# Kernel optimization log

Hardware: AMD Instinct MI355X
Metric: run time of the kernel (lower is better)

## Reference

```python
import jax, jax.numpy as jnp
import numpy as np

DIM = 256; H = 64; W = 64; NH = 8; NL = 1; NP = 8; HD = DIM // NH
B = 4


def _bilinear(img, grid):
    """torch.grid_sample(mode='bilinear', padding='zeros', align_corners=False).
    img: [C, Hl, Wl]; grid: [N, P, 2] normalized xy in [-1, 1]. Returns [C, N, P]."""
    Hl, Wl = img.shape[1], img.shape[2]
    x = (grid[..., 0] + 1.0) * (Wl * 0.5) - 0.5
    y = (grid[..., 1] + 1.0) * (Hl * 0.5) - 0.5
    x0 = jnp.floor(x); y0 = jnp.floor(y)
    wx = x - x0; wy = y - y0

    def gather(xi, yi):
        valid = (xi >= 0) & (xi < Wl) & (yi >= 0) & (yi < Hl)
        xc = jnp.clip(xi, 0, Wl - 1).astype(jnp.int32)
        yc = jnp.clip(yi, 0, Hl - 1).astype(jnp.int32)
        return img[:, yc, xc] * valid.astype(img.dtype)[None]  # [C, N, P]

    v00 = gather(x0, y0); v01 = gather(x0 + 1, y0)
    v10 = gather(x0, y0 + 1); v11 = gather(x0 + 1, y0 + 1)
    top = v00 * (1.0 - wx) + v01 * wx
    bot = v10 * (1.0 - wx) + v11 * wx
    return top * (1.0 - wy) + bot * wy


def _msda(value, loc, att):
    """multi_scale_deformable_attn_pytorch.
    value: [b, nv, NH, HD]; loc: [b, nq, NH, NL, NP, 2] in [0,1]; att: [b, nq, NH, NL, NP]."""
    b, nv, _, _ = value.shape
    nq = loc.shape[1]
    grids = 2.0 * loc - 1.0
    bn = b * NH
    level_shapes = [(H, W)] * NL  # all levels share the single [H, W] grid here
    sampled_levels = []
    offset = 0
    for l, (Hl, Wl) in enumerate(level_shapes):
        vl = value[:, offset:offset + Hl * Wl]                     # [b, HW, NH, HD]
        offset += Hl * Wl
        vl = vl.transpose(0, 2, 3, 1).reshape(bn, HD, Hl, Wl)      # [b*NH, HD, Hl, Wl]
        gl = grids[:, :, :, l].transpose(0, 2, 1, 3, 4).reshape(bn, nq, NP, 2)
        sampled_levels.append(jax.vmap(_bilinear)(vl, gl))         # [b*NH, HD, nq, NP]
    sampled = jnp.stack(sampled_levels, axis=3)                    # [b*NH, HD, nq, NL, NP]
    w = att.transpose(0, 2, 1, 3, 4).reshape(bn, 1, nq, NL, NP)
    out = jnp.sum(sampled * w, axis=(3, 4))                        # [b*NH, HD, nq]
    return out.reshape(b, NH, HD, nq).transpose(0, 3, 1, 2).reshape(b, nq, NH * HD)


def _forward(query, value, W_loc, b_loc, W_att, b_att, W_val, b_val, W_out, b_out):
    b = query.shape[0]
    nq = H * W
    q = query.transpose(0, 2, 3, 1).reshape(b, nq, DIM)
    v = value.transpose(0, 2, 3, 1).reshape(b, nq, DIM)
    loc = (q @ W_loc.T + b_loc).reshape(b, nq, NH, NL, NP, 2)
    att = jax.nn.softmax((q @ W_att.T + b_att).reshape(b, nq, NH, NL * NP), axis=-1)
    att = att.reshape(b, nq, NH, NL, NP)
    v = (v @ W_val.T + b_val).reshape(b, nq, NH, HD)
    out = _msda(v, loc, att)                                       # [b, nq, DIM]
    return out @ W_out.T + b_out


def setup_inputs() -> dict:
    key = jax.random.key(0)
    ks = jax.random.split(key, 12)
    s = 0.02
    return {
        "query": jax.random.normal(ks[0], (B, DIM, H, W), jnp.float32),
        "value": jax.random.normal(ks[1], (B, DIM, H, W), jnp.float32),
        "W_loc": jax.random.normal(ks[2], (NH * NL * NP * 2, DIM), jnp.float32) * s,
        "b_loc": jax.random.normal(ks[3], (NH * NL * NP * 2,), jnp.float32) * s,
        "W_att": jax.random.normal(ks[4], (NH * NL * NP, DIM), jnp.float32) * s,
        "b_att": jax.random.normal(ks[5], (NH * NL * NP,), jnp.float32) * s,
        "W_val": jax.random.normal(ks[6], (DIM, DIM), jnp.float32) * s,
        "b_val": jax.random.normal(ks[7], (DIM,), jnp.float32) * s,
        "W_out": jax.random.normal(ks[8], (DIM, DIM), jnp.float32) * s,
        "b_out": jax.random.normal(ks[9], (DIM,), jnp.float32) * s,
    }


def reference(query, value, W_loc, b_loc, W_att, b_att, W_val, b_val, W_out, b_out):
    return _forward(query, value, W_loc, b_loc, W_att, b_att, W_val, b_val, W_out, b_out)
```

## Files before the change

kernel.cpp:

```cpp
#include <hip/hip_runtime.h>
#include <hip/hip_bf16.h>
#include <math.h>

#define NQ   4096
#define DIMC 256
#define NHC  8
#define NPC  8
#define HDC  32
#define HC   64
#define WC   64
#define BC   4
#define LSTR 40

typedef __bf16 bf16x8 __attribute__((ext_vector_type(8)));
typedef __attribute__((ext_vector_type(4))) float f4;
typedef __attribute__((ext_vector_type(8))) short s8v;

__device__ __forceinline__ ushort f2bf(float f) {
  __hip_bfloat16 h = __float2bfloat16(f);
  union { __hip_bfloat16 h; ushort u; } c; c.h = h; return c.u;
}
__device__ __forceinline__ float bfu2f(ushort u) {
  union { unsigned i; float f; } c; c.i = ((unsigned)u) << 16; return c.f;
}
__device__ __forceinline__ float bflo(unsigned u) {
  union { unsigned i; float f; } c; c.i = u << 16; return c.f;
}
__device__ __forceinline__ float bfhi(unsigned u) {
  union { unsigned i; float f; } c; c.i = u & 0xffff0000u; return c.f;
}

union bfr8 { ushort u[8]; bf16x8 v; s8v s; };

__global__ __launch_bounds__(256) void k_proj(
    const float* __restrict__ query, const float* __restrict__ value,
    const float* __restrict__ W_loc, const float* __restrict__ b_loc,
    const float* __restrict__ W_att, const float* __restrict__ b_att,
    const float* __restrict__ W_val, const float* __restrict__ b_val,
    float* __restrict__ loc, float* __restrict__ att,
    ushort* __restrict__ vproj) {
  __shared__ __align__(16) ushort smem[4 * 64 * LSTR];
  const int tid = threadIdx.x;
  const int b = blockIdx.z, n0 = blockIdx.x * 64;
  const int lane = tid & 63, wid = tid >> 6;
  const int wn0 = (wid & 1) * 32, wo0 = (wid >> 1) * 32;
  const int am = lane & 15, kq = (lane >> 4) * 8;
  const int an = tid & 63, ak = (tid >> 6) * 8;
  const int wo = tid >> 2, wk = (tid & 3) * 8;

  f4 acc[2][2];
#pragma unroll
  for (int mi = 0; mi < 2; ++mi) { acc[mi][0] = (f4)0.f; acc[mi][1] = (f4)0.f; }

  if (blockIdx.y < 3) {
    ushort* Ah = smem;
    ushort* Al = smem + 64 * LSTR;
    ushort* Wh = smem + 2 * 64 * LSTR;
    ushort* Wl = smem + 3 * 64 * LSTR;
    const int o0 = blockIdx.y * 64;
    const float* Xb = query + (size_t)b * DIMC * NQ + n0 + an;
    const int oo = o0 + wo;
    const float* Wrow = (oo < 128) ? (W_loc + (size_t)oo * DIMC)
                                   : (W_att + (size_t)(oo - 128) * DIMC);
    float ax[8];
    float4 wx0, wx1;
#pragma unroll
    for (int j = 0; j < 8; ++j) ax[j] = Xb[(size_t)(ak + j) * NQ];
    wx0 = *(const float4*)(Wrow + wk);
    wx1 = *(const float4*)(Wrow + wk + 4);

    for (int t = 0; t < 8; ++t) {
      __syncthreads();
      {
        bfr8 ph, pl;
#pragma unroll
        for (int j = 0; j < 8; ++j) {
          ushort h = f2bf(ax[j]);
          ph.u[j] = h;
          pl.u[j] = f2bf(ax[j] - bfu2f(h));
        }
        *(s8v*)(&Ah[an * LSTR + ak]) = ph.s;
        *(s8v*)(&Al[an * LSTR + ak]) = pl.s;
        float wt[8] = {wx0.x, wx0.y, wx0.z, wx0.w, wx1.x, wx1.y, wx1.z, wx1.w};
        bfr8 qh, ql;
#pragma unroll
        for (int j = 0; j < 8; ++j) {
          ushort h = f2bf(wt[j]);
          qh.u[j] = h;
          ql.u[j] = f2bf(wt[j] - bfu2f(h));
        }
        *(s8v*)(&Wh[wo * LSTR + wk]) = qh.s;
        *(s8v*)(&Wl[wo * LSTR + wk]) = ql.s;
      }
      if (t < 7) {
        const int k0 = (t + 1) * 32;
#pragma unroll
        for (int j = 0; j < 8; ++j) ax[j] = Xb[(size_t)(k0 + ak + j) * NQ];
        wx0 = *(const float4*)(Wrow + k0 + wk);
        wx1 = *(const float4*)(Wrow + k0 + wk + 4);
      }
      __syncthreads();
      bf16x8 ah[2], al[2], bh[2], bl[2];
#pragma unroll
      for (int mi = 0; mi < 2; ++mi) {
        ah[mi] = *(const bf16x8*)(&Ah[(wn0 + mi * 16 + am) * LSTR + kq]);
        al[mi] = *(const bf16x8*)(&Al[(wn0 + mi * 16 + am) * LSTR + kq]);
      }
#pragma unroll
      for (int oj = 0; oj < 2; ++oj) {
        bh[oj] = *(const bf16x8*)(&Wh[(wo0 + oj * 16 + am) * LSTR + kq]);
        bl[oj] = *(const bf16x8*)(&Wl[(wo0 + oj * 16 + am) * LSTR + kq]);
      }
#pragma unroll
      for (int mi = 0; mi < 2; ++mi)
#pragma unroll
        for (int oj = 0; oj < 2; ++oj) {
          acc[mi][oj] = __builtin_amdgcn_mfma_f32_16x16x32_bf16(ah[mi], bh[oj], acc[mi][oj], 0, 0, 0);
          acc[mi][oj] = __builtin_amdgcn_mfma_f32_16x16x32_bf16(al[mi], bh[oj], acc[mi][oj], 0, 0, 0);
          acc[mi][oj] = __builtin_amdgcn_mfma_f32_16x16x32_bf16(ah[mi], bl[oj], acc[mi][oj], 0, 0, 0);
        }
    }
    const int o0l = blockIdx.y * 64;
    const bool isAtt = (o0l >= 128);
    float* dstBase = isAtt ? att : loc;
    const float* bias = isAtt ? b_att : b_loc;
    const int ostride = isAtt ? 64 : 128;
    const int ob = isAtt ? o0l - 128 : o0l;
#pragma unroll
    for (int oj = 0; oj < 2; ++oj) {
      const int o = ob + wo0 + oj * 16 + am;
      const float bv = bias[o];
#pragma unroll
      for (int mi = 0; mi < 2; ++mi) {
        const int nb = n0 + wn0 + mi * 16 + (lane >> 4) * 4;
#pragma unroll
        for (int r = 0; r < 4; ++r)
          dstBase[((size_t)b * NQ + nb + r) * ostride + o] = acc[mi][oj][r] + bv;
      }
    }
  } else {
    ushort* As = smem;
    ushort* Ws = smem + 64 * LSTR;
    const int o0 = (blockIdx.y - 3) * 64;
    const float* Xb = value + (size_t)b * DIMC * NQ + n0 + an;
    const float* Wrow = W_val + (size_t)(o0 + wo) * DIMC;

    float ax[8];
    float4 wx0, wx1;
#pragma unroll
    for (int j = 0; j < 8; ++j) ax[j] = Xb[(size_t)(ak + j) * NQ];
    wx0 = *(const float4*)(Wrow + wk);
    wx1 = *(const float4*)(Wrow + wk + 4);

    for (int t = 0; t < 8; ++t) {
      __syncthreads();
      {
        bfr8 pa;
#pragma unroll
        for (int j = 0; j < 8; ++j) pa.u[j] = f2bf(ax[j]);
        *(s8v*)(&As[an * LSTR + ak]) = pa.s;
        float wt[8] = {wx0.x, wx0.y, wx0.z, wx0.w, wx1.x, wx1.y, wx1.z, wx1.w};
        bfr8 pw;
#pragma unroll
        for (int j = 0; j < 8; ++j) pw.u[j] = f2bf(wt[j]);
        *(s8v*)(&Ws[wo * LSTR + wk]) = pw.s;
      }
      if (t < 7) {
        const int k0 = (t + 1) * 32;
#pragma unroll
        for (int j = 0; j < 8; ++j) ax[j] = Xb[(size_t)(k0 + ak + j) * NQ];
        wx0 = *(const float4*)(Wrow + k0 + wk);
        wx1 = *(const float4*)(Wrow + k0 + wk + 4);
      }
      __syncthreads();
      bf16x8 af[2], bf[2];
#pragma unroll
      for (int mi = 0; mi < 2; ++mi)
        af[mi] = *(const bf16x8*)(&As[(wn0 + mi * 16 + am) * LSTR + kq]);
#pragma unroll
      for (int oj = 0; oj < 2; ++oj)
        bf[oj] = *(const bf16x8*)(&Ws[(wo0 + oj * 16 + am) * LSTR + kq]);
#pragma unroll
      for (int mi = 0; mi < 2; ++mi)
#pragma unroll
        for (int oj = 0; oj < 2; ++oj)
          acc[mi][oj] = __builtin_amdgcn_mfma_f32_16x16x32_bf16(af[mi], bf[oj], acc[mi][oj], 0, 0, 0);
    }
#pragma unroll
    for (int oj = 0; oj < 2; ++oj) {
      const int o = o0 + wo0 + oj * 16 + am;
      const int h = o >> 5, d = o & 31;
      const float bias = b_val[o];
      ushort* dst = vproj + ((size_t)(b * NHC + h) * NQ) * HDC + d;
#pragma unroll
      for (int mi = 0; mi < 2; ++mi) {
        const int nb = n0 + wn0 + mi * 16 + (lane >> 4) * 4;
#pragma unroll
        for (int r = 0; r < 4; ++r)
          dst[(size_t)(nb + r) * HDC] = f2bf(acc[mi][oj][r] + bias);
      }
    }
  }
}

__global__ __launch_bounds__(256) void k_sample(
    const float* __restrict__ loc, const float* __restrict__ attL,
    const ushort* __restrict__ vproj, ushort* __restrict__ msda) {
  __shared__ float4 Lc[64][9];
  __shared__ int4   Lo[64][9];
  const int b = blockIdx.z, h = blockIdx.y;
  const int tid = threadIdx.x;
  const int n0 = blockIdx.x * 64;
#pragma unroll
  for (int it = 0; it < 2; ++it) {
    const int idx = it * 256 + tid;
    const int q = idx >> 3, p = idx & 7;
    const int n = n0 + q;
    const float lg = attL[((size_t)b * NQ + n) * 64 + h * 8 + p];
    float m = lg;
#pragma unroll
    for (int off = 1; off < 8; off <<= 1) m = fmaxf(m, __shfl_xor(m, off, 64));
    const float e = __expf(lg - m);
    float s = e;
#pragma unroll
    for (int off = 1; off < 8; off <<= 1) s += __shfl_xor(s, off, 64);
    const float w = e / s;
    const float2 xy = *(const float2*)(loc + ((size_t)b * NQ + n) * 128 + h * 16 + p * 2);
    const float x = xy.x * 64.0f - 0.5f;
    const float y = xy.y * 64.0f - 0.5f;
    const float x0f = floorf(x), y0f = floorf(y);
    const float wx = x - x0f, wy = y - y0f;
    const int x0 = (int)x0f, y0 = (int)y0f;
    const int x1 = x0 + 1, y1 = y0 + 1;
    const float fx0 = (x0 >= 0 && x0 < WC) ? 1.f : 0.f;
    const float fx1 = (x1 >= 0 && x1 < WC) ? 1.f : 0.f;
    const float fy0 = (y0 >= 0 && y0 < HC) ? 1.f : 0.f;
    const float fy1 = (y1 >= 0 && y1 < HC) ? 1.f : 0.f;
    const int cx0 = min(max(x0, 0), WC - 1), cx1 = min(max(x1, 0), WC - 1);
    const int cy0 = min(max(y0, 0), HC - 1), cy1 = min(max(y1, 0), HC - 1);
    float4 cf;
    cf.x = w * (1.f - wx) * (1.f - wy) * fx0 * fy0;
    cf.y = w * wx * (1.f - wy) * fx1 * fy0;
    cf.z = w * (1.f - wx) * wy * fx0 * fy1;
    cf.w = w * wx * wy * fx1 * fy1;
    int4 of;
    of.x = (cy0 * WC + cx0) * HDC; of.y = (cy0 * WC + cx1) * HDC;
    of.z = (cy1 * WC + cx0) * HDC; of.w = (cy1 * WC + cx1) * HDC;
    Lc[q][p] = cf; Lo[q][p] = of;
  }
  __syncthreads();
  const int q = tid >> 2, d8 = (tid & 3) * 8;
  const int n = n0 + q;
  const ushort* vb = vproj + (size_t)((b * NHC + h) * NQ) * HDC + d8;
  float a[8] = {};
#pragma unroll
  for (int p = 0; p < 8; ++p) {
    const int4 of = Lo[q][p];
    const float4 cf = Lc[q][p];
    const uint4 u00 = *(const uint4*)(vb + of.x);
    const uint4 u01 = *(const uint4*)(vb + of.y);
    const uint4 u10 = *(const uint4*)(vb + of.z);
    const uint4 u11 = *(const uint4*)(vb + of.w);
    const unsigned c00[4] = {u00.x, u00.y, u00.z, u00.w};
    const unsigned c01[4] = {u01.x, u01.y, u01.z, u01.w};
    const unsigned c10[4] = {u10.x, u10.y, u10.z, u10.w};
    const unsigned c11[4] = {u11.x, u11.y, u11.z, u11.w};
#pragma unroll
    for (int j = 0; j < 4; ++j) {
      a[2 * j]     += cf.x * bflo(c00[j]) + cf.y * bflo(c01[j]) + cf.z * bflo(c10[j]) + cf.w * bflo(c11[j]);
      a[2 * j + 1] += cf.x * bfhi(c00[j]) + cf.y * bfhi(c01[j]) + cf.z * bfhi(c10[j]) + cf.w * bfhi(c11[j]);
    }
  }
  bfr8 r;
#pragma unroll
  for (int j = 0; j < 8; ++j) r.u[j] = f2bf(a[j]);
  *(s8v*)(msda + ((size_t)b * NQ + n) * DIMC + h * HDC + d8) = r.s;
}

__global__ __launch_bounds__(256) void k_out(
    const ushort* __restrict__ msda, const float* __restrict__ W_out,
    const float* __restrict__ b_out, float* __restrict__ out) {
  __shared__ __align__(16) ushort As[64 * LSTR];
  __shared__ __align__(16) ushort Ws[64 * LSTR];
  const int b = blockIdx.z, n0 = blockIdx.x * 64, o0 = blockIdx.y * 64;
  const int tid = threadIdx.x, lane = tid & 63, wid = tid >> 6;
  const int wn0 = (wid & 1) * 32, wo0 = (wid >> 1) * 32;
  const int am = lane & 15, kq = (lane >> 4) * 8;
  const int ar = tid >> 2, akq = (tid & 3) * 8;
  const int wo = tid >> 2, wk = (tid & 3) * 8;
  const ushort* Ab = msda + ((size_t)b * NQ + n0 + ar) * DIMC + akq;
  const float* Wrow = W_out + (size_t)(o0 + wo) * DIMC;

  f4 acc[2][2];
#pragma unroll
  for (int mi = 0; mi < 2; ++mi) { acc[mi][0] = (f4)0.f; acc[mi][1] = (f4)0.f; }

  s8v aval = *(const s8v*)(Ab);
  float4 wx0 = *(const float4*)(Wrow + wk);
  float4 wx1 = *(const float4*)(Wrow + wk + 4);

  for (int t = 0; t < 8; ++t) {
    __syncthreads();
    *(s8v*)(&As[ar * LSTR + akq]) = aval;
    {
      float wt[8] = {wx0.x, wx0.y, wx0.z, wx0.w, wx1.x, wx1.y, wx1.z, wx1.w};
      bfr8 pw;
#pragma unroll
      for (int j = 0; j < 8; ++j) pw.u[j] = f2bf(wt[j]);
      *(s8v*)(&Ws[wo * LSTR + wk]) = pw.s;
    }
    if (t < 7) {
      const int k0 = (t + 1) * 32;
      aval = *(const s8v*)(Ab + k0);
      wx0 = *(const float4*)(Wrow + k0 + wk);
      wx1 = *(const float4*)(Wrow + k0 + wk + 4);
    }
    __syncthreads();
    bf16x8 af[2], bf[2];
#pragma unroll
    for (int mi = 0; mi < 2; ++mi)
      af[mi] = *(const bf16x8*)(&As[(wn0 + mi * 16 + am) * LSTR + kq]);
#pragma unroll
    for (int oj = 0; oj < 2; ++oj)
      bf[oj] = *(const bf16x8*)(&Ws[(wo0 + oj * 16 + am) * LSTR + kq]);
#pragma unroll
    for (int mi = 0; mi < 2; ++mi)
#pragma unroll
      for (int oj = 0; oj < 2; ++oj)
        acc[mi][oj] = __builtin_amdgcn_mfma_f32_16x16x32_bf16(af[mi], bf[oj], acc[mi][oj], 0, 0, 0);
  }
#pragma unroll
  for (int oj = 0; oj < 2; ++oj) {
    const int o = o0 + wo0 + oj * 16 + am;
    const float bias = b_out[o];
#pragma unroll
    for (int mi = 0; mi < 2; ++mi) {
      const int nb = n0 + wn0 + mi * 16 + (lane >> 4) * 4;
#pragma unroll
      for (int r = 0; r < 4; ++r)
        out[((size_t)b * NQ + nb + r) * DIMC + o] = acc[mi][oj][r] + bias;
    }
  }
}

extern "C" void kernel_launch(void* const* d_in, const int* in_sizes, int n_in,
                              void* d_out, int out_size, void* d_ws, size_t ws_size,
                              hipStream_t stream) {
  const float* query = (const float*)d_in[0];
  const float* value = (const float*)d_in[1];
  const float* W_loc = (const float*)d_in[2];
  const float* b_loc = (const float*)d_in[3];
  const float* W_att = (const float*)d_in[4];
  const float* b_att = (const float*)d_in[5];
  const float* W_val = (const float*)d_in[6];
  const float* b_val = (const float*)d_in[7];
  const float* W_out = (const float*)d_in[8];
  const float* b_out = (const float*)d_in[9];
  float* out = (float*)d_out;

  float* ws = (float*)d_ws;
  float* loc    = ws;
  float* att    = loc + (size_t)BC * NQ * 128;
  ushort* vproj = (ushort*)(att + (size_t)BC * NQ * 64);
  ushort* msda  = vproj + (size_t)BC * NHC * NQ * HDC;

  dim3 blk(256);
  k_proj  <<<dim3(NQ / 64, 7, BC), blk, 0, stream>>>(query, value, W_loc, b_loc,
             W_att, b_att, W_val, b_val, loc, att, vproj);
  k_sample<<<dim3(NQ / 64, NHC, BC), blk, 0, stream>>>(loc, att, vproj, msda);
  k_out   <<<dim3(NQ / 64, 4, BC), blk, 0, stream>>>(msda, W_out, b_out, out);
}
```

Baseline: 127.9 us.

## Fuse deformable sampling with output projection into one kernel via shared memory

Merges the sampling kernel and the output-projection GEMM into one kernel. Each block takes 32 queries across all 8 heads, keeps the sampled bf16 rows in shared memory and multiplies them by W_out directly, so the msda intermediate is no longer written to and re-read from global memory, and one launch is removed. Sampling is also restructured so each thread computes its own softmax and bilinear coefficients in registers instead of staging them through shared memory. In exchange, every block converts the full 256x256 W_out to bf16, which is redundant work across blocks, and the grid is smaller with fewer rows per block, which may hurt latency hiding in the gather phase.

Measured after the change: 160.3 us. +25.3%, slower.

```diff
diff --git a/kernel.cpp b/kernel.cpp
--- a/kernel.cpp
+++ b/kernel.cpp
@@ -11,6 +11,7 @@
 #define WC   64
 #define BC   4
 #define LSTR 40
+#define KSTR 264
 
 typedef __bf16 bf16x8 __attribute__((ext_vector_type(8)));
 typedef __attribute__((ext_vector_type(4))) float f4;
@@ -120,12 +121,11 @@
           acc[mi][oj] = __builtin_amdgcn_mfma_f32_16x16x32_bf16(ah[mi], bl[oj], acc[mi][oj], 0, 0, 0);
         }
     }
-    const int o0l = blockIdx.y * 64;
-    const bool isAtt = (o0l >= 128);
+    const bool isAtt = (o0 >= 128);
     float* dstBase = isAtt ? att : loc;
     const float* bias = isAtt ? b_att : b_loc;
     const int ostride = isAtt ? 64 : 128;
-    const int ob = isAtt ? o0l - 128 : o0l;
+    const int ob = isAtt ? o0 - 128 : o0;
 #pragma unroll
     for (int oj = 0; oj < 2; ++oj) {
       const int o = ob + wo0 + oj * 16 + am;
@@ -203,139 +203,140 @@
   }
 }
 
-__global__ __launch_bounds__(256) void k_sample(
+__global__ __launch_bounds__(256) void k_samout(
     const float* __restrict__ loc, const float* __restrict__ attL,
-    const ushort* __restrict__ vproj, ushort* __restrict__ msda) {
-  __shared__ float4 Lc[64][9];
-  __shared__ int4   Lo[64][9];
-  const int b = blockIdx.z, h = blockIdx.y;
-  const int tid = threadIdx.x;
-  const int n0 = blockIdx.x * 64;
-#pragma unroll
-  for (int it = 0; it < 2; ++it) {
-    const int idx = it * 256 + tid;
-    const int q = idx >> 3, p = idx & 7;
+    const ushort* __restrict__ vproj,
+    const float* __restrict__ W_out, const float* __restrict__ b_out,
+    float* __restrict__ out) {
+  __shared__ __align__(16) ushort As[32 * KSTR];
+  __shared__ __align__(16) ushort Ws[256 * LSTR];
+  const int tid = threadIdx.x, b = blockIdx.z, n0 = blockIdx.x * 32;
+
+#pragma unroll
+  for (int it = 0; it < 4; ++it) {
+    const int task = it * 256 + tid;
+    const int q = task >> 5, h = (task >> 2) & 7, dg = task & 3;
     const int n = n0 + q;
-    const float lg = attL[((size_t)b * NQ + n) * 64 + h * 8 + p];
-    float m = lg;
-#pragma unroll
-    for (int off = 1; off < 8; off <<= 1) m = fmaxf(m, __shfl_xor(m, off, 64));
-    const float e = __expf(lg - m);
-    float s = e;
-#pragma unroll
-    for (int off = 1; off < 8; off <<= 1) s += __shfl_xor(s, off, 64);
-    const float w = e / s;
-    const float2 xy = *(const float2*)(loc + ((size_t)b * NQ + n) * 128 + h * 16 + p * 2);
-    const float x = xy.x * 64.0f - 0.5f;
-    const float y = xy.y * 64.0f - 0.5f;
-    const float x0f = floorf(x), y0f = floorf(y);
-    const float wx = x - x0f, wy = y - y0f;
-    const int x0 = (int)x0f, y0 = (int)y0f;
-    const int x1 = x0 + 1, y1 = y0 + 1;
-    const float fx0 = (x0 >= 0 && x0 < WC) ? 1.f : 0.f;
-    const float fx1 = (x1 >= 0 && x1 < WC) ? 1.f : 0.f;
-    const float fy0 = (y0 >= 0 && y0 < HC) ? 1.f : 0.f;
-    const float fy1 = (y1 >= 0 && y1 < HC) ? 1.f : 0.f;
-    const int cx0 = min(max(x0, 0), WC - 1), cx1 = min(max(x1, 0), WC - 1);
-    const int cy0 = min(max(y0, 0), HC - 1), cy1 = min(max(y1, 0), HC - 1);
-    float4 cf;
-    cf.x = w * (1.f - wx) * (1.f - wy) * fx0 * fy0;
-    cf.y = w * wx * (1.f - wy) * fx1 * fy0;
-    cf.z = w * (1.f - wx) * wy * fx0 * fy1;
-    cf.w = w * wx * wy * fx1 * fy1;
-    int4 of;
-    of.x = (cy0 * WC + cx0) * HDC; of.y = (cy0 * WC + cx1) * HDC;
-    of.z = (cy1 * WC + cx0) * HDC; of.w = (cy1 * WC + cx1) * HDC;
-    Lc[q][p] = cf; Lo[q][p] = of;
+    const float* ap = attL + ((size_t)b * NQ + n) * 64 + h * 8;
+    const float4 l0 = *(const float4*)(ap);
+    const float4 l1 = *(const float4*)(ap + 4);
+    float lg[8] = {l0.x, l0.y, l0.z, l0.w, l1.x, l1.y, l1.z, l1.w};
+    float m = lg[0];
+#pragma unroll
+    for (int p = 1; p < 8; ++p) m = fmaxf(m, lg[p]);
+    float s = 0.f;
+#pragma unroll
+    for (int p = 0; p < 8; ++p) { lg[p] = __expf(lg[p] - m); s += lg[p]; }
+    const float inv = 1.0f / s;
+    const float* lp = loc + ((size_t)b * NQ + n) * 128 + h * 16;
+    float4 xy0 = *(const float4*)(lp);
+    float4 xy1 = *(const float4*)(lp + 4);
+    float4 xy2 = *(const float4*)(lp + 8);
+    float4 xy3 = *(const float4*)(lp + 12);
+    const float xyf[16] = {xy0.x, xy0.y, xy0.z, xy0.w, xy1.x, xy1.y, xy1.z, xy1.w,
+                           xy2.x, xy2.y, xy2.z, xy2.w, xy3.x, xy3.y, xy3.z, xy3.w};
+    const ushort* vb = vproj + ((size_t)(b * NHC + h) * NQ) * HDC + dg * 8;
+    float a[8] = {};
+#pragma unroll
+    for (int p = 0; p < 8; ++p) {
+      const float x = xyf[2 * p] * 64.0f - 0.5f;
+      const float y = xyf[2 * p + 1] * 64.0f - 0.5f;
+      const float x0f = floorf(x), y0f = floorf(y);
+      const float wx = x - x0f, wy = y - y0f;
+      const int x0 = (int)x0f, y0 = (int)y0f;
+      const int x1 = x0 + 1, y1 = y0 + 1;
+      const float fx0 = (x0 >= 0 && x0 < WC) ? 1.f : 0.f;
+      const float fx1 = (x1 >= 0 && x1 < WC) ? 1.f : 0.f;
+      const float fy0 = (y0 >= 0 && y0 < HC) ? 1.f : 0.f;
+      const float fy1 = (y1 >= 0 && y1 < HC) ? 1.f : 0.f;
+      const int cx0 = min(max(x0, 0), WC - 1), cx1 = min(max(x1, 0), WC - 1);
+      const int cy0 = min(max(y0, 0), HC - 1), cy1 = min(max(y1, 0), HC - 1);
+      const float w = lg[p] * inv;
+      const float c00 = w * (1.f - wx) * (1.f - wy) * fx0 * fy0;
+      const float c01 = w * wx * (1.f - wy) * fx1 * fy0;
+      const float c10 = w * (1.f - wx) * wy * fx0 * fy1;
+      const float c11 = w * wx * wy * fx1 * fy1;
+      const uint4 u00 = *(const uint4*)(vb + (cy0 * WC + cx0) * HDC);
+      const uint4 u01 = *(const uint4*)(vb + (cy0 * WC + cx1) * HDC);
+      const uint4 u10 = *(const uint4*)(vb + (cy1 * WC + cx0) * HDC);
+      const uint4 u11 = *(const uint4*)(vb + (cy1 * WC + cx1) * HDC);
+      const unsigned g00[4] = {u00.x, u00.y, u00.z, u00.w};
+      const unsigned g01[4] = {u01.x, u01.y, u01.z, u01.w};
+      const unsigned g10[4] = {u10.x, u10.y, u10.z, u10.w};
+      const unsigned g11[4] = {u11.x, u11.y, u11.z, u11.w};
+#pragma unroll
+      for (int j = 0; j < 4; ++j) {
+        a[2 * j]     += c00 * bflo(g00[j]) + c01 * bflo(g01[j]) + c10 * bflo(g10[j]) + c11 * bflo(g11[j]);
+        a[2 * j + 1] += c00 * bfhi(g00[j]) + c01 * bfhi(g01[j]) + c10 * bfhi(g10[j]) + c11 * bfhi(g11[j]);
+      }
+    }
+    bfr8 r;
+#pragma unroll
+    for (int j = 0; j < 8; ++j) r.u[j] = f2bf(a[j]);
+    *(s8v*)(&As[q * KSTR + h * 32 + dg * 8]) = r.s;
   }
-  __syncthreads();
-  const int q = tid >> 2, d8 = (tid & 3) * 8;
-  const int n = n0 + q;
-  const ushort* vb = vproj + (size_t)((b * NHC + h) * NQ) * HDC + d8;
-  float a[8] = {};
-#pragma unroll
-  for (int p = 0; p < 8; ++p) {
-    const int4 of = Lo[q][p];
-    const float4 cf = Lc[q][p];
-    const uint4 u00 = *(const uint4*)(vb + of.x);
-    const uint4 u01 = *(const uint4*)(vb + of.y);
-    const uint4 u10 = *(const uint4*)(vb + of.z);
-    const uint4 u11 = *(const uint4*)(vb + of.w);
-    const unsigned c00[4] = {u00.x, u00.y, u00.z, u00.w};
-    const unsigned c01[4] = {u01.x, u01.y, u01.z, u01.w};
-    const unsigned c10[4] = {u10.x, u10.y, u10.z, u10.w};
-    const unsigned c11[4] = {u11.x, u11.y, u11.z, u11.w};
-#pragma unroll
-    for (int j = 0; j < 4; ++j) {
-      a[2 * j]     += cf.x * bflo(c00[j]) + cf.y * bflo(c01[j]) + cf.z * bflo(c10[j]) + cf.w * bflo(c11[j]);
-      a[2 * j + 1] += cf.x * bfhi(c00[j]) + cf.y * bfhi(c01[j]) + cf.z * bfhi(c10[j]) + cf.w * bfhi(c11[j]);
-    }
-  }
-  bfr8 r;
-#pragma unroll
-  for (int j = 0; j < 8; ++j) r.u[j] = f2bf(a[j]);
-  *(s8v*)(msda + ((size_t)b * NQ + n) * DIMC + h * HDC + d8) = r.s;
-}
-
-__global__ __launch_bounds__(256) void k_out(
-    const ushort* __restrict__ msda, const float* __restrict__ W_out,
-    const float* __restrict__ b_out, float* __restrict__ out) {
-  __shared__ __align__(16) ushort As[64 * LSTR];
-  __shared__ __align__(16) ushort Ws[64 * LSTR];
-  const int b = blockIdx.z, n0 = blockIdx.x * 64, o0 = blockIdx.y * 64;
-  const int tid = threadIdx.x, lane = tid & 63, wid = tid >> 6;
-  const int wn0 = (wid & 1) * 32, wo0 = (wid >> 1) * 32;
-  const int am = lane & 15, kq = (lane >> 4) * 8;
-  const int ar = tid >> 2, akq = (tid & 3) * 8;
-  const int wo = tid >> 2, wk = (tid & 3) * 8;
-  const ushort* Ab = msda + ((size_t)b * NQ + n0 + ar) * DIMC + akq;
-  const float* Wrow = W_out + (size_t)(o0 + wo) * DIMC;
-
-  f4 acc[2][2];
-#pragma unroll
-  for (int mi = 0; mi < 2; ++mi) { acc[mi][0] = (f4)0.f; acc[mi][1] = (f4)0.f; }
-
-  s8v aval = *(const s8v*)(Ab);
-  float4 wx0 = *(const float4*)(Wrow + wk);
-  float4 wx1 = *(const float4*)(Wrow + wk + 4);
+
+  const int lane = tid & 63, wid = tid >> 6;
+  const int am = lane & 15, kq = (lane >> 4) * 8, row4 = (lane >> 4) * 4;
+  const int o0w = wid * 64;
+  const float* Wrow = W_out + (size_t)tid * DIMC;
+
+  float4 wx[8];
+#pragma unroll
+  for (int c = 0; c < 8; ++c) wx[c] = *(const float4*)(Wrow + c * 4);
+
+  f4 acc[2][4];
+#pragma unroll
+  for (int mi = 0; mi < 2; ++mi)
+#pragma unroll
+    for (int oj = 0; oj < 4; ++oj) acc[mi][oj] = (f4)0.f;
 
   for (int t = 0; t < 8; ++t) {
     __syncthreads();
-    *(s8v*)(&As[ar * LSTR + akq]) = aval;
     {
-      float wt[8] = {wx0.x, wx0.y, wx0.z, wx0.w, wx1.x, wx1.y, wx1.z, wx1.w};
-      bfr8 pw;
-#pragma unroll
-      for (int j = 0; j < 8; ++j) pw.u[j] = f2bf(wt[j]);
-      *(s8v*)(&Ws[wo * LSTR + wk]) = pw.s;
+      const float wt[32] = {wx[0].x, wx[0].y, wx[0].z, wx[0].w,
+                            wx[1].x, wx[1].y, wx[1].z, wx[1].w,
+                            wx[2].x, wx[2].y, wx[2].z, wx[2].w,
+                            wx[3].x, wx[3].y, wx[3].z, wx[3].w,
+                            wx[4].x, wx[4].y, wx[4].z, wx[4].w,
+                            wx[5].x, wx[5].y, wx[5].z, wx[5].w,
+                            wx[6].x, wx[6].y, wx[6].z, wx[6].w,
+                            wx[7].x, wx[7].y, wx[7].z, wx[7].w};
+      bfr8 pk[4];
+#pragma unroll
+      for (int g = 0; g < 4; ++g)
+#pragma unroll
+        for (int j = 0; j < 8; ++j) pk[g].u[j] = f2bf(wt[g * 8 + j]);
+#pragma unroll
+      for (int g = 0; g < 4; ++g)
+        *(s8v*)(&Ws[tid * LSTR + g * 8]) = pk[g].s;
     }
     if (t < 7) {
       const int k0 = (t + 1) * 32;
-      aval = *(const s8v*)(Ab + k0);
-      wx0 = *(const float4*)(Wrow + k0 + wk);
-      wx1 = *(const float4*)(Wrow + k0 + wk + 4);
+#pragma unroll
+      for (int c = 0; c < 8; ++c) wx[c] = *(const float4*)(Wrow + k0 + c * 4);
     }
     __syncthreads();
-    bf16x8 af[2], bf[2];
+    bf16x8 af[2], bf[4];
 #pragma unroll
     for (int mi = 0; mi < 2; ++mi)
-      af[mi] = *(const bf16x8*)(&As[(wn0 + mi * 16 + am) * LSTR + kq]);
-#pragma unroll
-    for (int oj = 0; oj < 2; ++oj)
-      bf[oj] = *(const bf16x8*)(&Ws[(wo0 + oj * 16 + am) * LSTR + kq]);
+      af[mi] = *(const bf16x8*)(&As[(mi * 16 + am) * KSTR + t * 32 + kq]);
+#pragma unroll
+    for (int oj = 0; oj < 4; ++oj)
+      bf[oj] = *(const bf16x8*)(&Ws[(o0w + oj * 16 + am) * LSTR + kq]);
 #pragma unroll
     for (int mi = 0; mi < 2; ++mi)
 #pragma unroll
-      for (int oj = 0; oj < 2; ++oj)
+      for (int oj = 0; oj < 4; ++oj)
         acc[mi][oj] = __builtin_amdgcn_mfma_f32_16x16x32_bf16(af[mi], bf[oj], acc[mi][oj], 0, 0, 0);
   }
 #pragma unroll
-  for (int oj = 0; oj < 2; ++oj) {
-    const int o = o0 + wo0 + oj * 16 + am;
+  for (int oj = 0; oj < 4; ++oj) {
+    const int o = o0w + oj * 16 + am;
     const float bias = b_out[o];
 #pragma unroll
     for (int mi = 0; mi < 2; ++mi) {
-      const int nb = n0 + wn0 + mi * 16 + (lane >> 4) * 4;
+      const int nb = n0 + mi * 16 + row4;
 #pragma unroll
       for (int r = 0; r < 4; ++r)
         out[((size_t)b * NQ + nb + r) * DIMC + o] = acc[mi][oj][r] + bias;
@@ -362,11 +363,10 @@
   float* loc    = ws;
   float* att    = loc + (size_t)BC * NQ * 128;
   ushort* vproj = (ushort*)(att + (size_t)BC * NQ * 64);
-  ushort* msda  = vproj + (size_t)BC * NHC * NQ * HDC;
 
   dim3 blk(256);
   k_proj  <<<dim3(NQ / 64, 7, BC), blk, 0, stream>>>(query, value, W_loc, b_loc,
              W_att, b_att, W_val, b_val, loc, att, vproj);
-  k_sample<<<dim3(NQ / 64, NHC, BC), blk, 0, stream>>>(loc, att, vproj, msda);
-  k_out   <<<dim3(NQ / 64, 4, BC), blk, 0, stream>>>(msda, W_out, b_out, out);
-}
+  k_samout<<<dim3(NQ / 32, 1, BC), blk, 0, stream>>>(loc, att, vproj,
+             W_out, b_out, out);
+}
```
